# Performance work log

Measured on AMD Instinct MI355X. Metric: run time of the kernel, lower is better.

The kernel has to match this reference:

```python
import jax, jax.numpy as jnp
import numpy as np

B, C, H, W = 4, 512, 64, 64
CH = C // 2  # 256


def setup_inputs() -> dict:
    key = jax.random.key(0)
    ks = jax.random.split(key, 10)
    s = 0.02  # keep logits in sane range for softmax
    return {
        "Fc": jax.random.normal(ks[0], (B, C, H, W), jnp.float32),
        "Fs": jax.random.normal(ks[1], (B, C, H, W), jnp.float32),
        "f_w": jax.random.normal(ks[2], (CH, C), jnp.float32) * s,
        "f_b": jax.random.normal(ks[3], (CH,), jnp.float32) * s,
        "g_w": jax.random.normal(ks[4], (CH, C), jnp.float32) * s,
        "g_b": jax.random.normal(ks[5], (CH,), jnp.float32) * s,
        "h_w": jax.random.normal(ks[6], (C, C), jnp.float32) * s,
        "h_b": jax.random.normal(ks[7], (C,), jnp.float32) * s,
        "out_w": jax.random.normal(ks[8], (C, C), jnp.float32) * s,
        "out_b": jax.random.normal(ks[9], (C,), jnp.float32) * s,
    }


def _conv1x1(x, w, b):
    # x: [B,C,H,W], w: [O,C], b: [O] -> [B,O,H,W]
    return jnp.einsum('oc,bchw->bohw', w, x) + b[None, :, None, None]


def reference(Fc, Fs, f_w, f_b, g_w, g_b, h_w, h_b, out_w, out_b):
    b, c, h, w = Fc.shape
    hw = h * w
    Ff = _conv1x1(Fc, f_w, f_b).reshape(b, -1, hw)   # [B, C/2, HW]
    Fg = _conv1x1(Fs, g_w, g_b).reshape(b, -1, hw)   # [B, C/2, HW]
    Fh = _conv1x1(Fs, h_w, h_b).reshape(b, -1, hw)   # [B, C,   HW]
    d_k = Ff.shape[1]  # channels//2, matches torch d_k after permute
    # Attention[b,i,j] over style positions j
    logits = jnp.einsum('bci,bcj->bij', Ff, Fg) / jnp.sqrt(jnp.float32(d_k))
    attn = jax.nn.softmax(logits, axis=-1)           # [B, HW, HW]
    # Out[b,c,i] = sum_j Fh[b,c,j] * attn[b,i,j]
    out = jnp.einsum('bcj,bij->bci', Fh, attn).reshape(b, c, h, w)
    return _conv1x1(out, out_w, out_b) + Fc
```

## Files before the change

### kernel.cpp

```cpp
#include <hip/hip_runtime.h>
#include <hip/hip_bf16.h>

#define HW    4096
#define CDIM  512
#define CHALF 256
#define NB    4
#define FLASH_LDS 50176
#define MERGE_LDS 66048

using bf16 = __hip_bfloat16;
typedef __attribute__((ext_vector_type(8))) short short8;
typedef __attribute__((ext_vector_type(4))) float float4v;

typedef __attribute__((address_space(1))) void gvoid_t;
typedef __attribute__((address_space(3))) void svoid_t;
#define GLD16(gp, lp) \
    __builtin_amdgcn_global_load_lds((gvoid_t*)(gp), (svoid_t*)(lp), 16, 0, 0)
#define MFMA(a, b, c) __builtin_amdgcn_mfma_f32_16x16x32_bf16(a, b, c, 0, 0, 0)

static __device__ __forceinline__ short8 ld_short8(const bf16* p) {
    return *reinterpret_cast<const short8*>(p);
}
static __device__ __forceinline__ float b2f(short s) {
    unsigned u = ((unsigned)(unsigned short)s) << 16;
    return __builtin_bit_cast(float, u);
}
static __device__ __forceinline__ short f2bs(float f) {
    bf16 h = __float2bfloat16(f);
    return __builtin_bit_cast(short, h);
}

__global__ void transpose_cast(const float* __restrict__ Fc,
                               const float* __restrict__ Fs,
                               bf16* __restrict__ FcT, bf16* __restrict__ FsT) {
    __shared__ float tile[32][33];
    int p0 = blockIdx.x * 32, c0 = blockIdx.y * 32;
    int z = blockIdx.z;
    int b = z & 3, which = z >> 2;
    const float* src = (which ? Fs : Fc) + (size_t)b * CDIM * HW;
    bf16* dst = (which ? FsT : FcT) + (size_t)b * HW * CDIM;
    int tx = threadIdx.x, ty = threadIdx.y;
    for (int i = 0; i < 4; i++)
        tile[ty + 8 * i][tx] = src[(size_t)(c0 + ty + 8 * i) * HW + p0 + tx];
    __syncthreads();
    for (int i = 0; i < 4; i++)
        dst[(size_t)(p0 + ty + 8 * i) * CDIM + c0 + tx] =
            __float2bfloat16(tile[tx][ty + 8 * i]);
}

__global__ void cast4(const float* __restrict__ fw, const float* __restrict__ gw,
                      const float* __restrict__ hw, const float* __restrict__ ow,
                      bf16* __restrict__ dst) {
    int i = blockIdx.x * 256 + threadIdx.x;
    float v;
    if (i < 131072)       v = fw[i] * 0.0625f;
    else if (i < 262144)  v = gw[i - 131072];
    else if (i < 524288)  v = hw[i - 262144];
    else                  v = ow[i - 524288];
    dst[i] = __float2bfloat16(v);
}

__launch_bounds__(256, 2)
__global__ void gemm_fg(const bf16* __restrict__ A1, const bf16* __restrict__ A2,
                        size_t sA,
                        const bf16* __restrict__ W1, const bf16* __restrict__ W2,
                        const float* __restrict__ b1, const float* __restrict__ b2,
                        float bs1, float bs2,
                        bf16* __restrict__ D1, bf16* __restrict__ D2, size_t sD,
                        int zhalf, int N, int K) {
    __shared__ bf16 Asf[2][8192];
    __shared__ bf16 Bsf[2][8192];
    int lid = blockIdx.x;
    int xcd = lid & 7, idx = lid >> 3;
    int bx = idx & 1;
    int yzg = xcd * 32 + (idx >> 1);
    int z = yzg >> 5;
    int by = yzg & 31;
    const bf16 *A, *W; const float* bias; float bsc; bf16* D;
    if (z < zhalf) { A = A1 + sA * z;           W = W1; bias = b1; bsc = bs1; D = D1 + sD * z; }
    else           { A = A2 + sA * (z - zhalf); W = W2; bias = b2; bsc = bs2; D = D2 + sD * (z - zhalf); }
    int m0 = by * 128, n0 = bx * 128;
    int t = threadIdx.x;
    int w = t >> 6, lane = t & 63;
    int wm = w >> 1, wn = w & 1;
    int l15 = lane & 15, quad = lane >> 4;
    int lr = lane >> 3, lc = (lane & 7) ^ lr;
    int nk = K >> 6;
    float4v acc[4][4] = {};

    for (int q = 0; q < 4; q++) {
        int rb = w * 32 + q * 8;
        GLD16(A + (size_t)(m0 + rb + lr) * K + lc * 8, &Asf[0][rb * 64]);
        GLD16(W + (size_t)(n0 + rb + lr) * K + lc * 8, &Bsf[0][rb * 64]);
    }
    for (int i = 0; i < nk; i++) {
        __syncthreads();
        if (i + 1 < nk) {
            int k0 = (i + 1) << 6, nb = (i + 1) & 1;
            for (int q = 0; q < 4; q++) {
                int rb = w * 32 + q * 8;
                GLD16(A + (size_t)(m0 + rb + lr) * K + k0 + lc * 8, &Asf[nb][rb * 64]);
                GLD16(W + (size_t)(n0 + rb + lr) * K + k0 + lc * 8, &Bsf[nb][rb * 64]);
            }
        }
        int cb = i & 1;
        for (int h = 0; h < 2; h++) {
            int p = (h * 4 + quad) ^ (l15 & 7);
            short8 af[4], bfr[4];
            for (int sm = 0; sm < 4; sm++)
                af[sm] = *(const short8*)&Asf[cb][(wm * 64 + sm * 16 + l15) * 64 + p * 8];
            for (int sn = 0; sn < 4; sn++)
                bfr[sn] = *(const short8*)&Bsf[cb][(wn * 64 + sn * 16 + l15) * 64 + p * 8];
            for (int sm = 0; sm < 4; sm++)
                for (int sn = 0; sn < 4; sn++)
                    acc[sm][sn] = MFMA(af[sm], bfr[sn], acc[sm][sn]);
        }
    }
    for (int sm = 0; sm < 4; sm++)
        for (int sn = 0; sn < 4; sn++) {
            int n = n0 + wn * 64 + sn * 16 + l15;
            for (int r = 0; r < 4; r++) {
                int m = m0 + wm * 64 + sm * 16 + quad * 4 + r;
                D[(size_t)m * N + n] = __float2bfloat16(acc[sm][sn][r] + bias[n] * bsc);
            }
        }
}

__launch_bounds__(256, 2)
__global__ void gemm_bw(const bf16* __restrict__ Aw,
                        const bf16* __restrict__ Bact, size_t sB,
                        const float* __restrict__ bias,
                        bf16* __restrict__ Dp, size_t sD,
                        int N, int K) {
    __shared__ bf16 Asf[2][8192];
    __shared__ bf16 Bsf[2][8192];
    int lid = blockIdx.x;
    int xcd = lid & 7, idx = lid >> 3;
    int my = idx & 3;
    int nzg = xcd * 16 + (idx >> 2);
    int z = nzg >> 5;
    int nx = nzg & 31;
    const bf16* A = Aw;
    const bf16* Bm = Bact + sB * z;
    int m0 = my * 128, n0 = nx * 128;
    int t = threadIdx.x;
    int w = t >> 6, lane = t & 63;
    int wm = w >> 1, wn = w & 1;
    int l15 = lane & 15, quad = lane >> 4;
    int lr = lane >> 3, lc = (lane & 7) ^ lr;
    int nk = K >> 6;
    float4v acc[4][4] = {};

    for (int q = 0; q < 4; q++) {
        int rb = w * 32 + q * 8;
        GLD16(A + (size_t)(m0 + rb + lr) * K + lc * 8, &Asf[0][rb * 64]);
        GLD16(Bm + (size_t)(n0 + rb + lr) * K + lc * 8, &Bsf[0][rb * 64]);
    }
    for (int i = 0; i < nk; i++) {
        __syncthreads();
        if (i + 1 < nk) {
            int k0 = (i + 1) << 6, nb = (i + 1) & 1;
            for (int q = 0; q < 4; q++) {
                int rb = w * 32 + q * 8;
                GLD16(A + (size_t)(m0 + rb + lr) * K + k0 + lc * 8, &Asf[nb][rb * 64]);
                GLD16(Bm + (size_t)(n0 + rb + lr) * K + k0 + lc * 8, &Bsf[nb][rb * 64]);
            }
        }
        int cb = i & 1;
        for (int h = 0; h < 2; h++) {
            int p = (h * 4 + quad) ^ (l15 & 7);
            short8 af[4], bfr[4];
            for (int sm = 0; sm < 4; sm++)
                af[sm] = *(const short8*)&Asf[cb][(wm * 64 + sm * 16 + l15) * 64 + p * 8];
            for (int sn = 0; sn < 4; sn++)
                bfr[sn] = *(const short8*)&Bsf[cb][(wn * 64 + sn * 16 + l15) * 64 + p * 8];
            for (int sm = 0; sm < 4; sm++)
                for (int sn = 0; sn < 4; sn++)
                    acc[sm][sn] = MFMA(af[sm], bfr[sn], acc[sm][sn]);
        }
    }
    for (int sm = 0; sm < 4; sm++)
        for (int sn = 0; sn < 4; sn++) {
            int n = n0 + wn * 64 + sn * 16 + l15;
            for (int r = 0; r < 4; r++) {
                int m = m0 + wm * 64 + sm * 16 + quad * 4 + r;
                Dp[sD * z + (size_t)m * N + n] =
                    __float2bfloat16(acc[sm][sn][r] + bias[m]);
            }
        }
}

__launch_bounds__(512, 1)
__global__ void flash_attn(const bf16* __restrict__ Q_, const bf16* __restrict__ Kt_,
                           const bf16* __restrict__ V_,
                           bf16* __restrict__ O0_, bf16* __restrict__ O1_,
                           float* __restrict__ L0_, float* __restrict__ L1_) {
    extern __shared__ char smem[];
    bf16* Ksf = (bf16*)smem;
    short* Ps = (short*)(smem + 32768);
    float* lpart = (float*)(smem + 49152);

    int lid = blockIdx.x;
    int stream = lid & 7;
    int b = stream & 3, jh = stream >> 2;
    int i0 = (lid >> 3) * 128;
    const bf16* Kt = Kt_ + (size_t)b * HW * CHALF;
    const bf16* V  = V_ + (size_t)b * CDIM * HW;
    bf16* Out   = (jh ? O1_ : O0_) + ((size_t)b * HW + i0) * CDIM;
    float* Lout = (jh ? L1_ : L0_) + (size_t)b * HW + i0;

    int t = threadIdx.x;
    int w = t >> 6, lane = t & 63;
    int l15 = lane & 15, quad = lane >> 4;
    int rm   = (w & 3) * 32;
    int cnw  = (w >> 2) * 32;
    int chb  = (w >> 2) * 4;
    int c0w  = w * 64;
    int jbeg = jh * (HW / 2), jend = jbeg + HW / 2;

    short8 qf0[8], qf1[8];
    {
        const bf16* qp = Q_ + ((size_t)b * HW + i0 + rm + l15) * CHALF + quad * 8;
        #pragma unroll
        for (int k8 = 0; k8 < 8; k8++) {
            qf0[k8] = ld_short8(qp + k8 * 32);
            qf1[k8] = ld_short8(qp + 16 * CHALF + k8 * 32);
        }
    }
    {
        int r0 = lane >> 5, cc = lane & 31;
        for (int i = 0; i < 4; i++) {
            int rp = i * 8 + w;
            int r = 2 * rp + r0;
            int c = cc ^ (r & 7);
            GLD16(Kt + (size_t)(jbeg + r) * CHALF + c * 8, &Ksf[rp * 512]);
        }
    }
    float l_lane[2][4] = {};
    float4v oacc[8][4] = {};
    __syncthreads();

    const bf16* vp = V + (size_t)(c0w + l15) * HW + quad * 8;
    for (int j0 = jbeg; j0 < jend; j0 += 64) {
        short8 va[4];
        #pragma unroll
        for (int sn = 0; sn < 4; sn++)
            va[sn] = ld_short8(vp + j0 + (size_t)(sn * 16) * HW);
        float4v s00 = {}, s01 = {}, s10 = {}, s11 = {};
        #pragma unroll
        for (int k8 = 0; k8 < 8; k8++) {
            int pq = ((k8 * 4 + quad) ^ (l15 & 7)) * 8;
            short8 k0 = *(const short8*)&Ksf[(cnw + l15) * 256 + pq];
            short8 k1 = *(const short8*)&Ksf[(cnw + 16 + l15) * 256 + pq];
            s00 = MFMA(qf0[k8], k0, s00);
            s01 = MFMA(qf0[k8], k1, s01);
            s10 = MFMA(qf1[k8], k0, s10);
            s11 = MFMA(qf1[k8], k1, s11);
        }
        #pragma unroll
        for (int r = 0; r < 4; r++) {
            int rl0 = rm + quad * 4 + r, rl1 = rl0 + 16;
            int cw = chb + (l15 >> 3);
            float p00 = __expf(s00[r]);
            float p01 = __expf(s01[r]);
            float p10 = __expf(s10[r]);
            float p11 = __expf(s11[r]);
            l_lane[0][r] += p00 + p01;
            l_lane[1][r] += p10 + p11;
            Ps[rl0 * 64 + ((cw + rl0) & 7) * 8 + (l15 & 7)]     = f2bs(p00);
            Ps[rl0 * 64 + ((cw + 2 + rl0) & 7) * 8 + (l15 & 7)] = f2bs(p01);
            Ps[rl1 * 64 + ((cw + rl1) & 7) * 8 + (l15 & 7)]     = f2bs(p10);
            Ps[rl1 * 64 + ((cw + 2 + rl1) & 7) * 8 + (l15 & 7)] = f2bs(p11);
        }
        __syncthreads();
        if (j0 + 64 < jend) {
            int r0 = lane >> 5, cc = lane & 31;
            for (int i = 0; i < 4; i++) {
                int rp = i * 8 + w;
                int r = 2 * rp + r0;
                int c = cc ^ (r & 7);
                GLD16(Kt + (size_t)(j0 + 64 + r) * CHALF + c * 8, &Ksf[rp * 512]);
            }
        }
        #pragma unroll
        for (int sm = 0; sm < 8; sm++) {
            int rl = sm * 16 + l15;
            short8 pf = *(const short8*)&Ps[rl * 64 + ((quad + rl) & 7) * 8];
            for (int sn = 0; sn < 4; sn++)
                oacc[sm][sn] = MFMA(pf, va[sn], oacc[sm][sn]);
        }
        short8 vb[4];
        #pragma unroll
        for (int sn = 0; sn < 4; sn++)
            vb[sn] = ld_short8(vp + j0 + 32 + (size_t)(sn * 16) * HW);
        #pragma unroll
        for (int sm = 0; sm < 8; sm++) {
            int rl = sm * 16 + l15;
            short8 pf = *(const short8*)&Ps[rl * 64 + ((4 + quad + rl) & 7) * 8];
            for (int sn = 0; sn < 4; sn++)
                oacc[sm][sn] = MFMA(pf, vb[sn], oacc[sm][sn]);
        }
        __syncthreads();
    }

    #pragma unroll
    for (int ms = 0; ms < 2; ms++)
        for (int r = 0; r < 4; r++) {
            float red = l_lane[ms][r];
            red += __shfl_xor(red, 1);
            red += __shfl_xor(red, 2);
            red += __shfl_xor(red, 4);
            red += __shfl_xor(red, 8);
            if (l15 == 0)
                lpart[(w >> 2) * 128 + rm + ms * 16 + quad * 4 + r] = red;
        }
    __syncthreads();
    if ((w >> 2) == 0 && l15 == 0)
        for (int ms = 0; ms < 2; ms++)
            for (int r = 0; r < 4; r++) {
                int rl = rm + ms * 16 + quad * 4 + r;
                Lout[rl] = lpart[rl] + lpart[128 + rl];
            }
    for (int sm = 0; sm < 8; sm++)
        for (int r = 0; r < 4; r++) {
            int rl = sm * 16 + quad * 4 + r;
            float li = 1.0f / (lpart[rl] + lpart[128 + rl]);
            for (int sn = 0; sn < 4; sn++)
                Out[(size_t)rl * CDIM + c0w + sn * 16 + l15] =
                    __float2bfloat16(oacc[sm][sn][r] * li);
        }
}

__launch_bounds__(256, 1)
__global__ void merge_out(const bf16* __restrict__ Op0, const bf16* __restrict__ Op1,
                          const float* __restrict__ L0, const float* __restrict__ L1,
                          const bf16* __restrict__ ow, const float* __restrict__ out_b,
                          const float* __restrict__ Fc, float* __restrict__ out) {
    extern __shared__ char smem[];
    short* Os = (short*)smem;
    float* lw = (float*)(smem + 65536);

    int rt = blockIdx.x;
    int b = rt >> 6;
    int i0 = (rt & 63) * 64;
    size_t obase = ((size_t)b * HW + i0) * CDIM;
    int t = threadIdx.x;

    if (t < 64) {
        float l0 = L0[(size_t)b * HW + i0 + t];
        float l1 = L1[(size_t)b * HW + i0 + t];
        float inv = 1.f / (l0 + l1);
        lw[t * 2] = l0 * inv;
        lw[t * 2 + 1] = l1 * inv;
    }
    __syncthreads();

    for (int q = 0; q < 16; q++) {
        int idx = q * 256 + t;
        int row = idx >> 6, cc = idx & 63;
        short8 a = ld_short8(Op0 + obase + (size_t)row * CDIM + cc * 8);
        short8 c = ld_short8(Op1 + obase + (size_t)row * CDIM + cc * 8);
        float w0 = lw[row * 2], w1 = lw[row * 2 + 1];
        short8 o;
        #pragma unroll
        for (int j = 0; j < 8; j++)
            o[j] = f2bs(w0 * b2f(a[j]) + w1 * b2f(c[j]));
        *(short8*)&Os[row * 512 + (cc ^ (row & 7)) * 8] = o;
    }
    __syncthreads();

    int w = t >> 6, lane = t & 63;
    int l15 = lane & 15, quad = lane >> 4;
    int m0 = w * 128;
    float4v acc[8][4] = {};
    for (int k8 = 0; k8 < 16; k8++) {
        short8 bfr[4];
        #pragma unroll
        for (int n16 = 0; n16 < 4; n16++)
            bfr[n16] = *(const short8*)&Os[(n16 * 16 + l15) * 512 +
                (((k8 * 4 + quad) ^ (l15 & 7))) * 8];
        short8 af[8];
        #pragma unroll
        for (int m16 = 0; m16 < 8; m16++)
            af[m16] = ld_short8(ow + (size_t)(m0 + m16 * 16 + l15) * CDIM +
                                k8 * 32 + quad * 8);
        #pragma unroll
        for (int m16 = 0; m16 < 8; m16++)
            for (int n16 = 0; n16 < 4; n16++)
                acc[m16][n16] = MFMA(af[m16], bfr[n16], acc[m16][n16]);
    }

    const float* fcb = Fc + (size_t)b * CDIM * HW;
    float* outb = out + (size_t)b * CDIM * HW;
    for (int m16 = 0; m16 < 8; m16++)
        for (int r = 0; r < 4; r++) {
            int co = m0 + m16 * 16 + quad * 4 + r;
            float bb = out_b[co];
            for (int n16 = 0; n16 < 4; n16++) {
                int i = i0 + n16 * 16 + l15;
                outb[(size_t)co * HW + i] =
                    acc[m16][n16][r] + bb + fcb[(size_t)co * HW + i];
            }
        }
}

extern "C" void kernel_launch(void* const* d_in, const int* in_sizes, int n_in,
                              void* d_out, int out_size, void* d_ws, size_t ws_size,
                              hipStream_t stream) {
    const float* Fc   = (const float*)d_in[0];
    const float* Fs   = (const float*)d_in[1];
    const float* f_w  = (const float*)d_in[2];
    const float* f_b  = (const float*)d_in[3];
    const float* g_w  = (const float*)d_in[4];
    const float* g_b  = (const float*)d_in[5];
    const float* h_w  = (const float*)d_in[6];
    const float* h_b  = (const float*)d_in[7];
    const float* out_w = (const float*)d_in[8];
    const float* out_b = (const float*)d_in[9];
    float* out = (float*)d_out;

    bf16* FcT = (bf16*)d_ws;
    bf16* FsT = FcT + (size_t)NB * HW * CDIM;
    bf16* FfT = FsT + (size_t)NB * HW * CDIM;
    bf16* FgT = FfT + (size_t)NB * HW * CHALF;
    bf16* Fh  = FgT + (size_t)NB * HW * CHALF;
    bf16* fw  = Fh  + (size_t)NB * CDIM * HW;
    bf16* gw  = fw + (size_t)CHALF * CDIM;
    bf16* hw  = gw + (size_t)CHALF * CDIM;
    bf16* ow  = hw + (size_t)CDIM * CDIM;
    float* L0 = (float*)(ow + (size_t)CDIM * CDIM);
    float* L1 = L0 + (size_t)NB * HW;
    bf16* Op0 = FcT;
    bf16* Op1 = FsT;

    hipFuncSetAttribute((const void*)flash_attn,
                        hipFuncAttributeMaxDynamicSharedMemorySize, FLASH_LDS);
    hipFuncSetAttribute((const void*)merge_out,
                        hipFuncAttributeMaxDynamicSharedMemorySize, MERGE_LDS);

    transpose_cast<<<dim3(HW / 32, CDIM / 32, NB * 2), dim3(32, 8), 0, stream>>>(
        Fc, Fs, FcT, FsT);
    cast4<<<dim3(786432 / 256), 256, 0, stream>>>(f_w, g_w, h_w, out_w, fw);

    gemm_fg<<<dim3(512), 256, 0, stream>>>(
        FcT, FsT, (size_t)HW * CDIM, fw, gw, f_b, g_b, 0.0625f, 1.0f,
        FfT, FgT, (size_t)HW * CHALF, NB, CHALF, CDIM);
    gemm_bw<<<dim3(512), 256, 0, stream>>>(
        hw, FsT, (size_t)HW * CDIM, h_b, Fh, (size_t)CDIM * HW, HW, CDIM);
    flash_attn<<<dim3(256), 512, FLASH_LDS, stream>>>(
        FfT, FgT, Fh, Op0, Op1, L0, L1);
    merge_out<<<dim3(256), 256, MERGE_LDS, stream>>>(
        Op0, Op1, L0, L1, ow, out_b, Fc, out);
}
```

Measured before the change: 399.5 us.

## Halve flash-attention query tile to 64 rows, 4 waves, two blocks per CU

The attention kernel now uses 64-row query tiles with 4 waves of 256 threads, and each wave covers 128 output channels instead of 64. The grid doubles to 512 blocks and launch bounds allow two blocks per CU. LDS drops because the P tile is smaller. MFMA sections are wrapped in s_setprio to favour matrix issue while the other block handles softmax and loads. In exchange each K tile is reused across fewer query rows, so K traffic and per-wave V loads grow.

```diff
diff --git a/kernel.cpp b/kernel.cpp
--- a/kernel.cpp
+++ b/kernel.cpp
@@ -5,7 +5,7 @@
 #define CDIM  512
 #define CHALF 256
 #define NB    4
-#define FLASH_LDS 50176
+#define FLASH_LDS 41472
 #define MERGE_LDS 66048
 
 using bf16 = __hip_bfloat16;
@@ -190,7 +190,7 @@
         }
 }
 
-__launch_bounds__(512, 1)
+__launch_bounds__(256, 2)
 __global__ void flash_attn(const bf16* __restrict__ Q_, const bf16* __restrict__ Kt_,
                            const bf16* __restrict__ V_,
                            bf16* __restrict__ O0_, bf16* __restrict__ O1_,
@@ -198,12 +198,12 @@
     extern __shared__ char smem[];
     bf16* Ksf = (bf16*)smem;
     short* Ps = (short*)(smem + 32768);
-    float* lpart = (float*)(smem + 49152);
+    float* lpart = (float*)(smem + 40960);
 
     int lid = blockIdx.x;
     int stream = lid & 7;
     int b = stream & 3, jh = stream >> 2;
-    int i0 = (lid >> 3) * 128;
+    int i0 = (lid >> 3) * 64;
     const bf16* Kt = Kt_ + (size_t)b * HW * CHALF;
     const bf16* V  = V_ + (size_t)b * CDIM * HW;
     bf16* Out   = (jh ? O1_ : O0_) + ((size_t)b * HW + i0) * CDIM;
@@ -212,10 +212,10 @@
     int t = threadIdx.x;
     int w = t >> 6, lane = t & 63;
     int l15 = lane & 15, quad = lane >> 4;
-    int rm   = (w & 3) * 32;
-    int cnw  = (w >> 2) * 32;
-    int chb  = (w >> 2) * 4;
-    int c0w  = w * 64;
+    int rm   = (w & 1) * 32;
+    int cnw  = (w >> 1) * 32;
+    int chb  = (w >> 1) * 4;
+    int c0w  = w * 128;
     int jbeg = jh * (HW / 2), jend = jbeg + HW / 2;
 
     short8 qf0[8], qf1[8];
@@ -229,24 +229,25 @@
     }
     {
         int r0 = lane >> 5, cc = lane & 31;
-        for (int i = 0; i < 4; i++) {
-            int rp = i * 8 + w;
+        for (int i = 0; i < 8; i++) {
+            int rp = i * 4 + w;
             int r = 2 * rp + r0;
             int c = cc ^ (r & 7);
             GLD16(Kt + (size_t)(jbeg + r) * CHALF + c * 8, &Ksf[rp * 512]);
         }
     }
     float l_lane[2][4] = {};
-    float4v oacc[8][4] = {};
+    float4v oacc[4][8] = {};
     __syncthreads();
 
     const bf16* vp = V + (size_t)(c0w + l15) * HW + quad * 8;
     for (int j0 = jbeg; j0 < jend; j0 += 64) {
-        short8 va[4];
+        short8 va0[4];
         #pragma unroll
         for (int sn = 0; sn < 4; sn++)
-            va[sn] = ld_short8(vp + j0 + (size_t)(sn * 16) * HW);
+            va0[sn] = ld_short8(vp + j0 + (size_t)(sn * 16) * HW);
         float4v s00 = {}, s01 = {}, s10 = {}, s11 = {};
+        __builtin_amdgcn_s_setprio(1);
         #pragma unroll
         for (int k8 = 0; k8 < 8; k8++) {
             int pq = ((k8 * 4 + quad) ^ (l15 & 7)) * 8;
@@ -257,6 +258,7 @@
             s10 = MFMA(qf1[k8], k0, s10);
             s11 = MFMA(qf1[k8], k1, s11);
         }
+        __builtin_amdgcn_s_setprio(0);
         #pragma unroll
         for (int r = 0; r < 4; r++) {
             int rl0 = rm + quad * 4 + r, rl1 = rl0 + 16;
@@ -275,31 +277,49 @@
         __syncthreads();
         if (j0 + 64 < jend) {
             int r0 = lane >> 5, cc = lane & 31;
-            for (int i = 0; i < 4; i++) {
-                int rp = i * 8 + w;
+            for (int i = 0; i < 8; i++) {
+                int rp = i * 4 + w;
                 int r = 2 * rp + r0;
                 int c = cc ^ (r & 7);
                 GLD16(Kt + (size_t)(j0 + 64 + r) * CHALF + c * 8, &Ksf[rp * 512]);
             }
         }
-        #pragma unroll
-        for (int sm = 0; sm < 8; sm++) {
+        short8 va1[4];
+        #pragma unroll
+        for (int sn = 0; sn < 4; sn++)
+            va1[sn] = ld_short8(vp + j0 + (size_t)(64 + sn * 16) * HW);
+        __builtin_amdgcn_s_setprio(1);
+        #pragma unroll
+        for (int sm = 0; sm < 4; sm++) {
             int rl = sm * 16 + l15;
             short8 pf = *(const short8*)&Ps[rl * 64 + ((quad + rl) & 7) * 8];
-            for (int sn = 0; sn < 4; sn++)
-                oacc[sm][sn] = MFMA(pf, va[sn], oacc[sm][sn]);
-        }
-        short8 vb[4];
-        #pragma unroll
-        for (int sn = 0; sn < 4; sn++)
-            vb[sn] = ld_short8(vp + j0 + 32 + (size_t)(sn * 16) * HW);
-        #pragma unroll
-        for (int sm = 0; sm < 8; sm++) {
+            #pragma unroll
+            for (int sn = 0; sn < 4; sn++)
+                oacc[sm][sn] = MFMA(pf, va0[sn], oacc[sm][sn]);
+            #pragma unroll
+            for (int sn = 0; sn < 4; sn++)
+                oacc[sm][4 + sn] = MFMA(pf, va1[sn], oacc[sm][4 + sn]);
+        }
+        __builtin_amdgcn_s_setprio(0);
+        short8 vb0[4], vb1[4];
+        #pragma unroll
+        for (int sn = 0; sn < 4; sn++) {
+            vb0[sn] = ld_short8(vp + j0 + 32 + (size_t)(sn * 16) * HW);
+            vb1[sn] = ld_short8(vp + j0 + 32 + (size_t)(64 + sn * 16) * HW);
+        }
+        __builtin_amdgcn_s_setprio(1);
+        #pragma unroll
+        for (int sm = 0; sm < 4; sm++) {
             int rl = sm * 16 + l15;
             short8 pf = *(const short8*)&Ps[rl * 64 + ((4 + quad + rl) & 7) * 8];
-            for (int sn = 0; sn < 4; sn++)
-                oacc[sm][sn] = MFMA(pf, vb[sn], oacc[sm][sn]);
-        }
+            #pragma unroll
+            for (int sn = 0; sn < 4; sn++)
+                oacc[sm][sn] = MFMA(pf, vb0[sn], oacc[sm][sn]);
+            #pragma unroll
+            for (int sn = 0; sn < 4; sn++)
+                oacc[sm][4 + sn] = MFMA(pf, vb1[sn], oacc[sm][4 + sn]);
+        }
+        __builtin_amdgcn_s_setprio(0);
         __syncthreads();
     }
 
@@ -312,22 +332,24 @@
             red += __shfl_xor(red, 4);
             red += __shfl_xor(red, 8);
             if (l15 == 0)
-                lpart[(w >> 2) * 128 + rm + ms * 16 + quad * 4 + r] = red;
+                lpart[(w >> 1) * 64 + rm + ms * 16 + quad * 4 + r] = red;
         }
     __syncthreads();
-    if ((w >> 2) == 0 && l15 == 0)
+    if ((w >> 1) == 0 && l15 == 0)
         for (int ms = 0; ms < 2; ms++)
             for (int r = 0; r < 4; r++) {
                 int rl = rm + ms * 16 + quad * 4 + r;
-                Lout[rl] = lpart[rl] + lpart[128 + rl];
-            }
-    for (int sm = 0; sm < 8; sm++)
+                Lout[rl] = lpart[rl] + lpart[64 + rl];
+            }
+    for (int sm = 0; sm < 4; sm++)
         for (int r = 0; r < 4; r++) {
             int rl = sm * 16 + quad * 4 + r;
-            float li = 1.0f / (lpart[rl] + lpart[128 + rl]);
-            for (int sn = 0; sn < 4; sn++)
-                Out[(size_t)rl * CDIM + c0w + sn * 16 + l15] =
+            float li = 1.0f / (lpart[rl] + lpart[64 + rl]);
+            for (int sn = 0; sn < 8; sn++) {
+                int ch = c0w + (sn >> 2) * 64 + (sn & 3) * 16 + l15;
+                Out[(size_t)rl * CDIM + ch] =
                     __float2bfloat16(oacc[sm][sn][r] * li);
+            }
         }
 }
 
@@ -447,7 +469,7 @@
         FfT, FgT, (size_t)HW * CHALF, NB, CHALF, CDIM);
     gemm_bw<<<dim3(512), 256, 0, stream>>>(
         hw, FsT, (size_t)HW * CDIM, h_b, Fh, (size_t)CDIM * HW, HW, CDIM);
-    flash_attn<<<dim3(256), 512, FLASH_LDS, stream>>>(
+    flash_attn<<<dim3(512), 256, FLASH_LDS, stream>>>(
         FfT, FgT, Fh, Op0, Op1, L0, L1);
     merge_out<<<dim3(256), 256, MERGE_LDS, stream>>>(
         Op0, Op1, L0, L1, ow, out_b, Fc, out);
```

Measured after the change: 539.0 us. 34.9% more time.
